# Kernel optimization log

Hardware: AMD Instinct MI355X
Metric: run time of the kernel (lower is better)

## Reference

```python
import jax, jax.numpy as jnp
import numpy as np

SEQ, BATCH, HIDDEN = 2048, 1, 4096
NUM_HEADS, NUM_KV_HEADS, HEAD_DIM = 32, 8, 128
Q_PER_GROUP = NUM_HEADS // NUM_KV_HEADS  # 4
TOTAL_PROJ = NUM_KV_HEADS * (Q_PER_GROUP + 2) * HEAD_DIM  # 6144


def setup_inputs() -> dict:
    key = jax.random.key(0)
    k1, k2, k3 = jax.random.split(key, 3)
    tokens = jax.random.normal(k1, (SEQ, BATCH, HIDDEN), dtype=jnp.float32)
    # xavier-ish scaling so activations stay sane
    weight_qkv = jax.random.normal(k2, (TOTAL_PROJ, HIDDEN), dtype=jnp.float32) * (2.0 / (TOTAL_PROJ + HIDDEN)) ** 0.5
    weight_proj = jax.random.normal(k3, (HIDDEN, NUM_HEADS * HEAD_DIM), dtype=jnp.float32) * (2.0 / (HIDDEN + NUM_HEADS * HEAD_DIM)) ** 0.5
    return {"tokens": tokens, "weight_qkv": weight_qkv, "weight_proj": weight_proj}


def reference(tokens, weight_qkv, weight_proj):
    S, B, H = tokens.shape
    scale = 1.0 / HEAD_DIM ** 0.5
    # QKV projection with interleaved GQA layout: per KV group [q0..q_{g-1}, k, v]
    qkv = jnp.einsum('sbh,ph->sbp', tokens, weight_qkv)
    qkv = qkv.reshape(S, B, NUM_KV_HEADS, Q_PER_GROUP + 2, HEAD_DIM)
    q = qkv[:, :, :, :Q_PER_GROUP, :].reshape(S, B, NUM_HEADS, HEAD_DIM)
    k = qkv[:, :, :, Q_PER_GROUP, :]       # [S,B,KVH,D]
    v = qkv[:, :, :, Q_PER_GROUP + 1, :]
    # repeat_interleave KV heads to match Q heads (GQA)
    k = jnp.repeat(k, Q_PER_GROUP, axis=2)
    v = jnp.repeat(v, Q_PER_GROUP, axis=2)
    # [S,B,H,D] -> [B,H,S,D]
    q = q.transpose(1, 2, 0, 3)
    k = k.transpose(1, 2, 0, 3)
    v = v.transpose(1, 2, 0, 3)
    scores = jnp.einsum('bhsd,bhtd->bhst', q, k) * scale
    causal = jnp.tril(jnp.ones((S, S), dtype=bool))
    scores = jnp.where(causal, scores, jnp.finfo(scores.dtype).min)
    attn = jax.nn.softmax(scores, axis=-1)
    out = jnp.einsum('bhst,bhtd->bhsd', attn, v)
    # [B,H,S,D] -> [S,B,H*D]
    out = out.transpose(2, 0, 1, 3).reshape(S, B, NUM_HEADS * HEAD_DIM)
    return jnp.einsum('sbe,he->sbh', out, weight_proj)
```

## Files before the change

kernel.cpp:

```cpp
#include <hip/hip_runtime.h>
#include <hip/hip_bf16.h>
#include <stdint.h>

#define SEQ 2048
#define HIDDEN 4096
#define NHEADS 32
#define HD 128
#define QKV_LD 6144
#define OUT_LD 4096

typedef __attribute__((ext_vector_type(8))) short short8;
typedef __attribute__((ext_vector_type(4))) short short4v;
typedef __attribute__((ext_vector_type(4))) float f32x4;
typedef __attribute__((ext_vector_type(4))) int int4v;
typedef __attribute__((ext_vector_type(2))) unsigned int uint2v;
typedef __attribute__((ext_vector_type(4))) float float4v;

__device__ __forceinline__ short f2bf(float f) {
  uint32_t u = __builtin_bit_cast(uint32_t, f);
  u += 0x7fff + ((u >> 16) & 1);
  return (short)(u >> 16);
}

__global__ void cast_kernel(const float* __restrict__ in, short* __restrict__ out, int n4) {
  int stride = gridDim.x * blockDim.x;
  for (int i = blockIdx.x * blockDim.x + threadIdx.x; i < n4; i += stride) {
    float4v v = ((const float4v*)in)[i];
    short4v o;
    o[0] = f2bf(v[0]); o[1] = f2bf(v[1]); o[2] = f2bf(v[2]); o[3] = f2bf(v[3]);
    ((short4v*)out)[i] = o;
  }
}

template <typename OT, int NBF>
__global__ __launch_bounds__(512, 4) void gemm128(const short* __restrict__ A,
                                                  const short* __restrict__ B,
                                                  OT* __restrict__ C,
                                                  int M, int N, int K, int NT) {
  __shared__ __align__(16) short lds[16384 + NBF * 8192];
  const int tid = threadIdx.x;
  const int w = tid >> 6, lane = tid & 63;
  const int wr = w >> 2, wc = w & 3;
  const int llo = lane & 15, lhi = lane >> 4;

  const int xcd = (int)blockIdx.x & 7;
  const int i = (int)blockIdx.x >> 3;
  const int nt = xcd * (NT >> 3) + (i >> 4);
  const int mt = i & 15;
  const size_t arow0 = (size_t)mt * 128, brow0 = (size_t)nt * (NBF * 64);
  const short* Ab = A + arow0 * K;
  const short* Bb = B + brow0 * K;

  f32x4 acc[4][NBF] = {};

  auto STAGE_A = [&](int kt, int j) {
    const int bufd = kt & 1;
    const int r0 = (j << 6) + (w << 3);
    const int row = r0 + (lane >> 3);
    const short* src = Ab + (size_t)row * K + (kt << 6) + (((lane & 7) ^ (row & 7)) << 3);
    short* dst = lds + (bufd << 13) + r0 * 64;
    __builtin_amdgcn_global_load_lds(
        (const __attribute__((address_space(1))) uint32_t*)src,
        (__attribute__((address_space(3))) uint32_t*)dst, 16, 0, 0);
  };
  auto STAGE_B = [&](int kt, int j) {
    const int bufd = kt & 1;
    const int r0 = (j << 6) + (w << 3);
    const int row = r0 + (lane >> 3);
    const short* src = Bb + (size_t)row * K + (kt << 6) + (((lane & 7) ^ (row & 7)) << 3);
    short* dst = lds + 16384 + bufd * (NBF << 12) + r0 * 64;
    __builtin_amdgcn_global_load_lds(
        (const __attribute__((address_space(1))) uint32_t*)src,
        (__attribute__((address_space(3))) uint32_t*)dst, 16, 0, 0);
  };
  auto STAGE = [&](int kt) {
#pragma unroll
    for (int j = 0; j < 2; j++) STAGE_A(kt, j);
#pragma unroll
    for (int j = 0; j < NBF; j++) STAGE_B(kt, j);
  };

  auto LDA = [&](int bufd, int m, int kk) -> short8 {
    const int row = (wr << 6) + (m << 4) + llo;
    const int ch = ((kk << 2) + lhi) ^ (row & 7);
    return *(const short8*)(lds + (bufd << 13) + row * 64 + (ch << 3));
  };
  auto LDB = [&](int bufd, int n, int kk) -> short8 {
    const int row = wc * (NBF << 4) + (n << 4) + llo;
    const int ch = ((kk << 2) + lhi) ^ (row & 7);
    return *(const short8*)(lds + 16384 + bufd * (NBF << 12) + row * 64 + (ch << 3));
  };

  STAGE(0);
  STAGE(1);
  if constexpr (NBF == 3) asm volatile("s_waitcnt vmcnt(5)" ::: "memory");
  else                    asm volatile("s_waitcnt vmcnt(4)" ::: "memory");
  __builtin_amdgcn_s_barrier();

  const int NKT = K >> 6;
  for (int kt = 0; kt < NKT; ++kt) {
    const int bufd = kt & 1;
    short8 b_[NBF][2];
#pragma unroll
    for (int n = 0; n < NBF; n++) { b_[n][0] = LDB(bufd, n, 0); b_[n][1] = LDB(bufd, n, 1); }
#pragma unroll
    for (int m = 0; m < 4; m++) {
      short8 a0 = LDA(bufd, m, 0);
      short8 a1 = LDA(bufd, m, 1);
#pragma unroll
      for (int n = 0; n < NBF; n++) {
        acc[m][n] = __builtin_amdgcn_mfma_f32_16x16x32_bf16(a0, b_[n][0], acc[m][n], 0, 0, 0);
        acc[m][n] = __builtin_amdgcn_mfma_f32_16x16x32_bf16(a1, b_[n][1], acc[m][n], 0, 0, 0);
      }
    }
    asm volatile("s_waitcnt lgkmcnt(0)" ::: "memory");
    __builtin_amdgcn_s_barrier();
    if (kt + 2 < NKT) STAGE(kt + 2);
    if (kt + 1 < NKT) {
      if (kt + 2 < NKT) {
        if constexpr (NBF == 3) asm volatile("s_waitcnt vmcnt(5)" ::: "memory");
        else                    asm volatile("s_waitcnt vmcnt(4)" ::: "memory");
      } else {
        asm volatile("s_waitcnt vmcnt(0)" ::: "memory");
      }
      __builtin_amdgcn_s_barrier();
    }
  }

#pragma unroll
  for (int m = 0; m < 4; m++)
#pragma unroll
    for (int n = 0; n < NBF; n++)
#pragma unroll
      for (int r = 0; r < 4; r++) {
        const size_t row = arow0 + (wr << 6) + (m << 4) + (lhi << 2) + r;
        const size_t col = brow0 + wc * (NBF << 4) + (n << 4) + llo;
        const float v = acc[m][n][r];
        if constexpr (sizeof(OT) == 2) C[row * N + col] = f2bf(v);
        else                           C[row * N + col] = v;
      }
}

__global__ __launch_bounds__(512) void attn_fwd(const short* __restrict__ qkv,
                                                short* __restrict__ aout) {
  const int qt = gridDim.y - 1 - blockIdx.y;
  const int h = blockIdx.x;
  const int kvh = h >> 2, g = h & 3;
  const int tid = threadIdx.x;
  const int wave = tid >> 6, lane = tid & 63;
  const int lhi = lane >> 4, llo = lane & 15;

  __shared__ __align__(16) short Ksm[2][128 * 128];
  __shared__ __align__(16) short Vsm[128 * 128];
  __shared__ __align__(16) short Psm[8][16 * 136];

  const float scale2 = 0.08838834764831845f * 1.4426950408889634f;

  const int qrow = qt * 128 + wave * 16 + llo;
  const short* qbase = qkv + (size_t)qrow * QKV_LD + (kvh * 6 + g) * HD;
  short8 qf[4];
#pragma unroll
  for (int kk = 0; kk < 4; kk++) qf[kk] = *(const short8*)(qbase + kk * 32 + lhi * 8);

  f32x4 o[8] = {};
  float mrow[4], lrow[4];
#pragma unroll
  for (int r = 0; r < 4; r++) { mrow[r] = -1e30f; lrow[r] = 0.f; }

  const short* Kg = qkv + (kvh * 6 + 4) * HD;
  const short* Vg = qkv + (kvh * 6 + 5) * HD;

  auto STAGE_K = [&](int t, int buf) {
#pragma unroll
    for (int c = 0; c < 4; c++) {
      const int call = wave * 4 + c;
      const int row = call * 4 + lhi;
      const int sc = llo ^ (row & 7);
      __builtin_amdgcn_global_load_lds(
          (const __attribute__((address_space(1))) uint32_t*)(Kg + (size_t)(t * 128 + row) * QKV_LD + sc * 8),
          (__attribute__((address_space(3))) uint32_t*)(&Ksm[buf][0] + call * 512), 16, 0, 0);
    }
  };
  short8 vreg[4];
  auto LOAD_V = [&](int t) {
#pragma unroll
    for (int c = 0; c < 4; c++) {
      const int idx = c * 512 + tid;
      const int vr = idx >> 4;
      vreg[c] = *(const short8*)(Vg + (size_t)(t * 128 + vr) * QKV_LD + (idx & 15) * 8);
    }
  };
  auto WRITE_V = [&]() {
#pragma unroll
    for (int c = 0; c < 4; c++) {
      const int idx = c * 512 + tid;
      const int vr = idx >> 4, vc = idx & 15;
      *(short8*)(&Vsm[0] + ((vr >> 2) * 8 + (vc >> 1)) * 64 + (vr & 3) * 16 + (vc & 1) * 8) = vreg[c];
    }
  };

  const uint32_t vlane0 = (uint32_t)(uintptr_t)(__attribute__((address_space(3))) short*)(&Vsm[0])
                          + (uint32_t)(lhi * 2048 + llo * 8);

  STAGE_K(0, 0);
  LOAD_V(0);
  asm volatile("s_waitcnt vmcnt(0)" ::: "memory");
  WRITE_V();
  __syncthreads();

  const int ntiles = qt + 1;
  const int qpos0 = qt * 128 + wave * 16 + lhi * 4;
  for (int t = 0; t < ntiles; t++) {
    const int cur = t & 1, nxt = cur ^ 1;
    const bool pf = (t + 1 < ntiles);
    if (pf) { LOAD_V(t + 1); STAGE_K(t + 1, nxt); }

    const short* Kc = &Ksm[cur][0];
    f32x4 s[8] = {};
#pragma unroll
    for (int n = 0; n < 8; n++) {
#pragma unroll
      for (int kk = 0; kk < 4; kk++) {
        const int krow = n * 16 + llo;
        const int ch = (kk * 4 + lhi) ^ (krow & 7);
        short8 kf = *(const short8*)(Kc + krow * 128 + ch * 8);
        s[n] = __builtin_amdgcn_mfma_f32_16x16x32_bf16(qf[kk], kf, s[n], 0, 0, 0);
      }
    }

    float sv[8][4];
    if (t == qt) {
#pragma unroll
      for (int n = 0; n < 8; n++)
#pragma unroll
        for (int r = 0; r < 4; r++) {
          float x = s[n][r] * scale2;
          if (t * 128 + n * 16 + llo > qpos0 + r) x = -1e30f;
          sv[n][r] = x;
        }
    } else {
#pragma unroll
      for (int n = 0; n < 8; n++)
#pragma unroll
        for (int r = 0; r < 4; r++) sv[n][r] = s[n][r] * scale2;
    }

    float rm4[4];
#pragma unroll
    for (int r = 0; r < 4; r++) {
      float rm = sv[0][r];
#pragma unroll
      for (int n = 1; n < 8; n++) rm = fmaxf(rm, sv[n][r]);
#pragma unroll
      for (int msk = 1; msk < 16; msk <<= 1) rm = fmaxf(rm, __shfl_xor(rm, msk));
      rm4[r] = rm;
    }
    bool need = false;
#pragma unroll
    for (int r = 0; r < 4; r++) need = need || (rm4[r] > mrow[r] + 8.0f);
    if (__any(need)) {
#pragma unroll
      for (int r = 0; r < 4; r++) {
        const float mnew = fmaxf(mrow[r], rm4[r]);
        const float a = exp2f(mrow[r] - mnew);
        mrow[r] = mnew;
        lrow[r] *= a;
#pragma unroll
        for (int nn = 0; nn < 8; nn++) o[nn][r] *= a;
      }
    }
#pragma unroll
    for (int r = 0; r < 4; r++) {
      float rs = 0.f;
#pragma unroll
      for (int n = 0; n < 8; n++) {
        float p = exp2f(sv[n][r] - mrow[r]);
        sv[n][r] = p;
        rs += p;
      }
#pragma unroll
      for (int msk = 1; msk < 16; msk <<= 1) rs += __shfl_xor(rs, msk);
      lrow[r] += rs;
    }

    short* P = &Psm[wave][0];
#pragma unroll
    for (int n = 0; n < 8; n++)
#pragma unroll
      for (int r = 0; r < 4; r++)
        P[(lhi * 4 + r) * 136 + n * 16 + llo] = f2bf(sv[n][r]);
    short8 pa[4];
#pragma unroll
    for (int ks = 0; ks < 4; ks++)
      pa[ks] = *(const short8*)(P + llo * 136 + ks * 32 + lhi * 8);

#pragma unroll
    for (int ks = 0; ks < 4; ks++) {
      uint2v vr_[8][2];
#pragma unroll
      for (int nn = 0; nn < 8; nn++)
#pragma unroll
        for (int hh = 0; hh < 2; hh++) {
          asm volatile("ds_read_b64_tr_b16 %0, %1 offset:%2"
                       : "=v"(vr_[nn][hh])
                       : "v"(vlane0), "i"(ks * 8192 + hh * 1024 + nn * 128));
        }
      asm volatile("s_waitcnt lgkmcnt(0)" ::: "memory");
      __builtin_amdgcn_sched_barrier(0);
#pragma unroll
      for (int nn = 0; nn < 8; nn++) {
        int4v tv;
        tv[0] = (int)vr_[nn][0][0]; tv[1] = (int)vr_[nn][0][1];
        tv[2] = (int)vr_[nn][1][0]; tv[3] = (int)vr_[nn][1][1];
        o[nn] = __builtin_amdgcn_mfma_f32_16x16x32_bf16(pa[ks], __builtin_bit_cast(short8, tv), o[nn], 0, 0, 0);
      }
    }

    if (pf) {
      __syncthreads();
      WRITE_V();
      __syncthreads();
    }
  }

#pragma unroll
  for (int nn = 0; nn < 8; nn++)
#pragma unroll
    for (int r = 0; r < 4; r++) {
      const size_t row = qt * 128 + wave * 16 + lhi * 4 + r;
      const size_t col = (size_t)h * HD + nn * 16 + llo;
      aout[row * OUT_LD + col] = f2bf(o[nn][r] / lrow[r]);
    }
}

extern "C" void kernel_launch(void* const* d_in, const int* in_sizes, int n_in,
                              void* d_out, int out_size, void* d_ws, size_t ws_size,
                              hipStream_t stream) {
  const float* tokens = (const float*)d_in[0];
  const float* wqkv   = (const float*)d_in[1];
  const float* wproj  = (const float*)d_in[2];
  float* out = (float*)d_out;

  short* tok_bf   = (short*)d_ws;
  short* wqkv_bf  = tok_bf   + (size_t)SEQ * HIDDEN;
  short* wproj_bf = wqkv_bf  + (size_t)QKV_LD * HIDDEN;
  short* qkv_bf   = wproj_bf + (size_t)HIDDEN * OUT_LD;
  short* attn_bf  = qkv_bf   + (size_t)SEQ * QKV_LD;

  cast_kernel<<<2048, 256, 0, stream>>>(tokens, tok_bf, SEQ * HIDDEN / 4);
  cast_kernel<<<2048, 256, 0, stream>>>(wqkv, wqkv_bf, QKV_LD * HIDDEN / 4);
  cast_kernel<<<2048, 256, 0, stream>>>(wproj, wproj_bf, HIDDEN * OUT_LD / 4);

  gemm128<short, 3><<<512, 512, 0, stream>>>(tok_bf, wqkv_bf, qkv_bf, SEQ, QKV_LD, HIDDEN, QKV_LD / 192);

  attn_fwd<<<dim3(NHEADS, SEQ / 128), 512, 0, stream>>>(qkv_bf, attn_bf);

  gemm128<float, 2><<<512, 512, 0, stream>>>(attn_bf, wproj_bf, out, SEQ, OUT_LD, HIDDEN, OUT_LD / 128);
}
```

Baseline: 311.3 us.

## Use 256-row tile GEMM with double-buffered direct-to-LDS loads for output projection

Adds a new GEMM kernel that computes 256x128 output tiles per block, where each wave handles 128 rows. K-tiles are double-buffered in LDS through global_load_lds with XOR swizzling, and the kernel uses an XCD-aware tile mapping. The output projection now launches 256 blocks instead of 512, which raises operand reuse per block and cuts global traffic. In exchange it uses more accumulator registers and LDS per block and has fewer blocks to fill the CUs.

```diff
diff --git a/kernel.cpp b/kernel.cpp
--- a/kernel.cpp
+++ b/kernel.cpp
@@ -141,6 +141,115 @@
       }
 }
 
+template <typename OT, int NBF>
+__global__ __launch_bounds__(512, 2) void gemm256b(const short* __restrict__ A,
+                                                   const short* __restrict__ B,
+                                                   OT* __restrict__ C,
+                                                   int M, int N, int K, int NT) {
+  __shared__ __align__(16) short lds[32768 + NBF * 8192];
+  const int tid = threadIdx.x;
+  const int w = tid >> 6, lane = tid & 63;
+  const int wr = w >> 2, wc = w & 3;
+  const int llo = lane & 15, lhi = lane >> 4;
+
+  const int xcd = (int)blockIdx.x & 7;
+  const int i = (int)blockIdx.x >> 3;
+  const int nt = xcd * (NT >> 3) + (i >> 3);
+  const int mt = i & 7;
+  const size_t arow0 = (size_t)mt * 256, brow0 = (size_t)nt * (NBF * 64);
+  const short* Ab = A + arow0 * K;
+  const short* Bb = B + brow0 * K;
+
+  f32x4 acc[8][NBF] = {};
+
+  auto STAGE_A = [&](int kt, int j) {
+    const int bufd = kt & 1;
+    const int r0 = (j << 6) + (w << 3);
+    const int row = r0 + (lane >> 3);
+    const short* src = Ab + (size_t)row * K + (kt << 6) + (((lane & 7) ^ (row & 7)) << 3);
+    short* dst = lds + (bufd << 14) + r0 * 64;
+    __builtin_amdgcn_global_load_lds(
+        (const __attribute__((address_space(1))) uint32_t*)src,
+        (__attribute__((address_space(3))) uint32_t*)dst, 16, 0, 0);
+  };
+  auto STAGE_B = [&](int kt, int j) {
+    const int bufd = kt & 1;
+    const int r0 = (j << 6) + (w << 3);
+    const int row = r0 + (lane >> 3);
+    const short* src = Bb + (size_t)row * K + (kt << 6) + (((lane & 7) ^ (row & 7)) << 3);
+    short* dst = lds + 32768 + bufd * (NBF << 12) + r0 * 64;
+    __builtin_amdgcn_global_load_lds(
+        (const __attribute__((address_space(1))) uint32_t*)src,
+        (__attribute__((address_space(3))) uint32_t*)dst, 16, 0, 0);
+  };
+  auto STAGE = [&](int kt) {
+#pragma unroll
+    for (int j = 0; j < 4; j++) STAGE_A(kt, j);
+#pragma unroll
+    for (int j = 0; j < NBF; j++) STAGE_B(kt, j);
+  };
+
+  auto LDA = [&](int bufd, int m, int kk) -> short8 {
+    const int row = (wr << 7) + (m << 4) + llo;
+    const int ch = ((kk << 2) + lhi) ^ (row & 7);
+    return *(const short8*)(lds + (bufd << 14) + row * 64 + (ch << 3));
+  };
+  auto LDB = [&](int bufd, int n, int kk) -> short8 {
+    const int row = wc * (NBF << 4) + (n << 4) + llo;
+    const int ch = ((kk << 2) + lhi) ^ (row & 7);
+    return *(const short8*)(lds + 32768 + bufd * (NBF << 12) + row * 64 + (ch << 3));
+  };
+
+  STAGE(0);
+  STAGE(1);
+  if constexpr (NBF == 3) asm volatile("s_waitcnt vmcnt(7)" ::: "memory");
+  else                    asm volatile("s_waitcnt vmcnt(6)" ::: "memory");
+  __builtin_amdgcn_s_barrier();
+
+  const int NKT = K >> 6;
+  for (int kt = 0; kt < NKT; ++kt) {
+    const int bufd = kt & 1;
+    short8 b_[NBF][2];
+#pragma unroll
+    for (int n = 0; n < NBF; n++) { b_[n][0] = LDB(bufd, n, 0); b_[n][1] = LDB(bufd, n, 1); }
+#pragma unroll
+    for (int m = 0; m < 8; m++) {
+      short8 a0 = LDA(bufd, m, 0);
+      short8 a1 = LDA(bufd, m, 1);
+#pragma unroll
+      for (int n = 0; n < NBF; n++) {
+        acc[m][n] = __builtin_amdgcn_mfma_f32_16x16x32_bf16(a0, b_[n][0], acc[m][n], 0, 0, 0);
+        acc[m][n] = __builtin_amdgcn_mfma_f32_16x16x32_bf16(a1, b_[n][1], acc[m][n], 0, 0, 0);
+      }
+    }
+    asm volatile("s_waitcnt lgkmcnt(0)" ::: "memory");
+    __builtin_amdgcn_s_barrier();
+    if (kt + 2 < NKT) STAGE(kt + 2);
+    if (kt + 1 < NKT) {
+      if (kt + 2 < NKT) {
+        if constexpr (NBF == 3) asm volatile("s_waitcnt vmcnt(7)" ::: "memory");
+        else                    asm volatile("s_waitcnt vmcnt(6)" ::: "memory");
+      } else {
+        asm volatile("s_waitcnt vmcnt(0)" ::: "memory");
+      }
+      __builtin_amdgcn_s_barrier();
+    }
+  }
+
+#pragma unroll
+  for (int m = 0; m < 8; m++)
+#pragma unroll
+    for (int n = 0; n < NBF; n++)
+#pragma unroll
+      for (int r = 0; r < 4; r++) {
+        const size_t row = arow0 + (wr << 7) + (m << 4) + (lhi << 2) + r;
+        const size_t col = brow0 + wc * (NBF << 4) + (n << 4) + llo;
+        const float v = acc[m][n][r];
+        if constexpr (sizeof(OT) == 2) C[row * N + col] = f2bf(v);
+        else                           C[row * N + col] = v;
+      }
+}
+
 __global__ __launch_bounds__(512) void attn_fwd(const short* __restrict__ qkv,
                                                 short* __restrict__ aout) {
   const int qt = gridDim.y - 1 - blockIdx.y;
@@ -355,5 +464,5 @@
 
   attn_fwd<<<dim3(NHEADS, SEQ / 128), 512, 0, stream>>>(qkv_bf, attn_bf);
 
-  gemm128<float, 2><<<512, 512, 0, stream>>>(attn_bf, wproj_bf, out, SEQ, OUT_LD, HIDDEN, OUT_LD / 128);
-}
+  gemm256b<float, 2><<<256, 512, 0, stream>>>(attn_bf, wproj_bf, out, SEQ, OUT_LD, HIDDEN, OUT_LD / 128);
+}
```

New measurement: 314.3 us. No clear change (+1.0%).
